# Performance work log

Measured on AMD Instinct MI355X. Metric: run time of the kernel, lower is better.

Reference implementation:

```python
import jax, jax.numpy as jnp
import numpy as np

NUM_QUBITS = 12
BOND_DIM = 8
DIM = 2 ** NUM_QUBITS  # 4096


def setup_inputs() -> dict:
    key = jax.random.key(0)
    k0, k1, k2, k3 = jax.random.split(key, 4)
    core0 = jax.random.normal(k0, (2, BOND_DIM), dtype=jnp.float32) * 0.5
    cores_mid = jax.random.normal(k1, (NUM_QUBITS - 2, BOND_DIM, 2, BOND_DIM), dtype=jnp.float32) * 0.5
    core_last = jax.random.normal(k2, (BOND_DIM, 2), dtype=jnp.float32) * 0.5
    A = jax.random.normal(k3, (DIM, DIM), dtype=jnp.float32)
    H = 0.5 * (A + A.T)  # Hamiltonians are symmetric
    return {"core0": core0, "cores_mid": cores_mid, "core_last": core_last, "H": H}


def _build_state(core0, cores_mid, core_last):
    # Sequential MPS contraction: state grows (2^k, D) site by site.
    state = core0  # (2, D)
    n_mid = cores_mid.shape[0]
    D = core0.shape[1]
    for i in range(n_mid):  # fixed, small layer loop (not a data-dim loop)
        # (S, a) x (a, p, b) -> (S, p, b) -> (S*2, b)
        state = jnp.einsum('sa,apb->spb', state, cores_mid[i]).reshape(-1, D)
    # (S, a) x (a, p) -> flat state vector of length 2^n
    psi = jnp.einsum('sa,ap->sp', state, core_last).reshape(-1)
    return psi


def reference(core0, cores_mid, core_last, H):
    psi = _build_state(core0, cores_mid, core_last)  # (2^n,)
    norm = jnp.dot(psi, psi)
    hpsi = H @ psi
    energy = jnp.dot(psi, hpsi) / norm          # <psi|H|psi>/<psi|psi>
    e2 = jnp.dot(psi, H @ hpsi) / norm          # <psi|H^2|psi>/<psi|psi>
    variance = jnp.maximum(e2 - energy * energy, 0.0)
    return jnp.stack([energy, variance])
```

## Files before the change

kernel.cpp:

```cpp
#include <hip/hip_runtime.h>
#include <hip/hip_bf16.h>


#define DIM 4096
#define BOND 8
#define NMID 10
#define T 128
#define NT (DIM / T)
#define NPAIRS (NT * (NT + 1) / 2)


__global__ __launch_bounds__(256) void build_psi_kernel(
    const float* __restrict__ core0,
    const float* __restrict__ cores_mid,
    const float* __restrict__ core_last,
    float* __restrict__ psi_g,
    float* __restrict__ hpsi_g) {
  __shared__ float c0[16];
  __shared__ float cm[NMID * 128];
  __shared__ float cl[16];

  if (threadIdx.x < 16) {
    c0[threadIdx.x] = core0[threadIdx.x];
    cl[threadIdx.x] = core_last[threadIdx.x];
  }
  for (int j = threadIdx.x; j < NMID * 128; j += 256) cm[j] = cores_mid[j];
  __syncthreads();

  const int idx = blockIdx.x * 256 + threadIdx.x;
  hpsi_g[idx] = 0.f;

  float v[BOND], nv[BOND];
  const int s0 = (idx >> 11) & 1;
#pragma unroll
  for (int a = 0; a < BOND; a++) v[a] = c0[s0 * BOND + a];

#pragma unroll
  for (int i = 0; i < NMID; i++) {
    const int p = (idx >> (10 - i)) & 1;
    const float* M = &cm[i * 128 + p * BOND];
#pragma unroll
    for (int b = 0; b < BOND; b++) nv[b] = v[0] * M[b];
#pragma unroll
    for (int a = 1; a < BOND; a++) {
#pragma unroll
      for (int b = 0; b < BOND; b++) nv[b] += v[a] * M[a * 16 + b];
    }
#pragma unroll
    for (int a = 0; a < BOND; a++) v[a] = nv[a];
  }

  const int pl = idx & 1;
  float ps = 0.f;
#pragma unroll
  for (int a = 0; a < BOND; a++) ps += v[a] * cl[a * 2 + pl];

  psi_g[idx] = ps;
}

__global__ __launch_bounds__(256) void symv_kernel(
    const float* __restrict__ H,
    const float* __restrict__ psi_g,
    float* __restrict__ hpsi_g) {
  int rem = blockIdx.x;
  int bi = 0;
  while (rem >= NT - bi) { rem -= (NT - bi); ++bi; }
  const int bj = bi + rem;
  const bool diag = (bi == bj);

  __shared__ float xI[T], xJ[T], yI_s[T], yJp[4 * T];

  if (threadIdx.x < T) {
    xI[threadIdx.x] = psi_g[bi * T + threadIdx.x];
    xJ[threadIdx.x] = psi_g[bj * T + threadIdx.x];
  }
  __syncthreads();

  const int wave = threadIdx.x >> 6;
  const int lane = threadIdx.x & 63;
  const float* __restrict__ base = H + (size_t)(bi * T) * DIM + bj * T;

  float aJx = 0.f, aJy = 0.f;
  const float pJx = xJ[lane * 2], pJy = xJ[lane * 2 + 1];

#pragma unroll 4
  for (int k = 0; k < T / 4; ++k) {
    const int r = k * 4 + wave;
    const float2 a = *reinterpret_cast<const float2*>(base + (size_t)r * DIM + lane * 2);
    const float xr = xI[r];
    aJx += a.x * xr;
    aJy += a.y * xr;
    float d = a.x * pJx + a.y * pJy;
#pragma unroll
    for (int off = 32; off > 0; off >>= 1) d += __shfl_down(d, off, 64);
    if (lane == 0) yI_s[r] = d;
  }

  yJp[wave * T + lane * 2] = aJx;
  yJp[wave * T + lane * 2 + 1] = aJy;
  __syncthreads();

  if (threadIdx.x < T) {
    atomicAdd(&hpsi_g[bi * T + threadIdx.x], yI_s[threadIdx.x]);
    if (!diag) {
      const float yj = yJp[threadIdx.x] + yJp[T + threadIdx.x] +
                       yJp[2 * T + threadIdx.x] + yJp[3 * T + threadIdx.x];
      atomicAdd(&hpsi_g[bj * T + threadIdx.x], yj);
    }
  }
}

__global__ __launch_bounds__(256) void dots_kernel(
    const float* __restrict__ psi_g,
    const float* __restrict__ hpsi_g,
    float* __restrict__ out) {
  __shared__ double s_n[4], s_ph[4], s_hh[4];
  double n = 0.0, ph = 0.0, hh = 0.0;
  for (int i = threadIdx.x; i < DIM; i += 256) {
    const double p = (double)psi_g[i];
    const double h = (double)hpsi_g[i];
    n += p * p;
    ph += p * h;
    hh += h * h;
  }
#pragma unroll
  for (int off = 32; off > 0; off >>= 1) {
    n += __shfl_down(n, off, 64);
    ph += __shfl_down(ph, off, 64);
    hh += __shfl_down(hh, off, 64);
  }
  const int wave = threadIdx.x >> 6;
  const int lane = threadIdx.x & 63;
  if (lane == 0) { s_n[wave] = n; s_ph[wave] = ph; s_hh[wave] = hh; }
  __syncthreads();
  if (threadIdx.x == 0) {
    double N = 0.0, P = 0.0, HH = 0.0;
#pragma unroll
    for (int w = 0; w < 4; w++) { N += s_n[w]; P += s_ph[w]; HH += s_hh[w]; }
    const double e = P / N;
    const double e2 = HH / N;
    double var = e2 - e * e;
    if (var < 0.0) var = 0.0;
    out[0] = (float)e;
    out[1] = (float)var;
  }
}

extern "C" void kernel_launch(void* const* d_in, const int* in_sizes, int n_in,
                              void* d_out, int out_size, void* d_ws, size_t ws_size,
                              hipStream_t stream) {
  const float* core0 = (const float*)d_in[0];
  const float* cores_mid = (const float*)d_in[1];
  const float* core_last = (const float*)d_in[2];
  const float* H = (const float*)d_in[3];

  float* psi = (float*)d_ws;
  float* hpsi = psi + DIM;

  build_psi_kernel<<<DIM / 256, 256, 0, stream>>>(core0, cores_mid, core_last, psi, hpsi);
  symv_kernel<<<NPAIRS, 256, 0, stream>>>(H, psi, hpsi);
  dots_kernel<<<1, 256, 0, stream>>>(psi, hpsi, (float*)d_out);
}
```

Before: 123.4 us.

## Fuse state build, symmetric matvec and reductions into one cooperative kernel

Merges the three kernels (MPS state build, blocked symmetric matvec, final dot reductions) into a single cooperative launch separated by grid-wide syncs. Each tile block recomputes the psi slices it needs in registers instead of reading them from global memory, and diagonal blocks write psi and zero hpsi. The aim is to remove two kernel launch gaps and the global round trip for psi. In exchange it adds cooperative-launch overhead, grid barrier costs, and redundant psi computation per block.

```diff
diff --git a/kernel.cpp b/kernel.cpp
--- a/kernel.cpp
+++ b/kernel.cpp
@@ -1,5 +1,7 @@
 #include <hip/hip_runtime.h>
-#include <hip/hip_bf16.h>
+#include <hip/hip_cooperative_groups.h>
+
+namespace cg = cooperative_groups;
 
 
 #define DIM 4096
@@ -9,16 +11,25 @@
 #define NT (DIM / T)
 #define NPAIRS (NT * (NT + 1) / 2)
 
-
-__global__ __launch_bounds__(256) void build_psi_kernel(
+__global__ __launch_bounds__(256, 3) void fused_vqe_kernel(
     const float* __restrict__ core0,
     const float* __restrict__ cores_mid,
     const float* __restrict__ core_last,
+    const float* __restrict__ H,
     float* __restrict__ psi_g,
-    float* __restrict__ hpsi_g) {
-  __shared__ float c0[16];
-  __shared__ float cm[NMID * 128];
-  __shared__ float cl[16];
+    float* __restrict__ hpsi_g,
+    float* __restrict__ out) {
+  cg::grid_group grid = cg::this_grid();
+
+  __shared__ float c0[16], cm[NMID * 128], cl[16];
+  __shared__ float xI[T], xJ[T], yI_s[T], yJp[4 * T];
+  __shared__ double sred[12];
+
+  int rem = blockIdx.x;
+  int bi = 0;
+  while (rem >= NT - bi) { rem -= (NT - bi); ++bi; }
+  const int bj = bi + rem;
+  const bool diag = (bi == bj);
 
   if (threadIdx.x < 16) {
     c0[threadIdx.x] = core0[threadIdx.x];
@@ -27,54 +38,43 @@
   for (int j = threadIdx.x; j < NMID * 128; j += 256) cm[j] = cores_mid[j];
   __syncthreads();
 
-  const int idx = blockIdx.x * 256 + threadIdx.x;
-  hpsi_g[idx] = 0.f;
+  {
+    const int local = threadIdx.x & 127;
+    const int slice = (threadIdx.x < 128) ? bi : bj;
+    const int idx = slice * T + local;
 
-  float v[BOND], nv[BOND];
-  const int s0 = (idx >> 11) & 1;
+    float v[BOND], nv[BOND];
+    const int s0 = (idx >> 11) & 1;
 #pragma unroll
-  for (int a = 0; a < BOND; a++) v[a] = c0[s0 * BOND + a];
+    for (int a = 0; a < BOND; a++) v[a] = c0[s0 * BOND + a];
+#pragma unroll
+    for (int i = 0; i < NMID; i++) {
+      const int p = (idx >> (10 - i)) & 1;
+      const float* M = &cm[i * 128 + p * BOND];
+#pragma unroll
+      for (int b = 0; b < BOND; b++) nv[b] = v[0] * M[b];
+#pragma unroll
+      for (int a = 1; a < BOND; a++) {
+#pragma unroll
+        for (int b = 0; b < BOND; b++) nv[b] += v[a] * M[a * 16 + b];
+      }
+#pragma unroll
+      for (int a = 0; a < BOND; a++) v[a] = nv[a];
+    }
+    const int pl = idx & 1;
+    float ps = 0.f;
+#pragma unroll
+    for (int a = 0; a < BOND; a++) ps += v[a] * cl[a * 2 + pl];
 
-#pragma unroll
-  for (int i = 0; i < NMID; i++) {
-    const int p = (idx >> (10 - i)) & 1;
-    const float* M = &cm[i * 128 + p * BOND];
-#pragma unroll
-    for (int b = 0; b < BOND; b++) nv[b] = v[0] * M[b];
-#pragma unroll
-    for (int a = 1; a < BOND; a++) {
-#pragma unroll
-      for (int b = 0; b < BOND; b++) nv[b] += v[a] * M[a * 16 + b];
+    if (threadIdx.x < 128) xI[local] = ps; else xJ[local] = ps;
+
+    if (diag && threadIdx.x < 128) {
+      psi_g[idx] = ps;
+      hpsi_g[idx] = 0.f;
     }
-#pragma unroll
-    for (int a = 0; a < BOND; a++) v[a] = nv[a];
-  }
-
-  const int pl = idx & 1;
-  float ps = 0.f;
-#pragma unroll
-  for (int a = 0; a < BOND; a++) ps += v[a] * cl[a * 2 + pl];
-
-  psi_g[idx] = ps;
-}
-
-__global__ __launch_bounds__(256) void symv_kernel(
-    const float* __restrict__ H,
-    const float* __restrict__ psi_g,
-    float* __restrict__ hpsi_g) {
-  int rem = blockIdx.x;
-  int bi = 0;
-  while (rem >= NT - bi) { rem -= (NT - bi); ++bi; }
-  const int bj = bi + rem;
-  const bool diag = (bi == bj);
-
-  __shared__ float xI[T], xJ[T], yI_s[T], yJp[4 * T];
-
-  if (threadIdx.x < T) {
-    xI[threadIdx.x] = psi_g[bi * T + threadIdx.x];
-    xJ[threadIdx.x] = psi_g[bj * T + threadIdx.x];
   }
   __syncthreads();
+  grid.sync();
 
   const int wave = threadIdx.x >> 6;
   const int lane = threadIdx.x & 63;
@@ -108,41 +108,36 @@
       atomicAdd(&hpsi_g[bj * T + threadIdx.x], yj);
     }
   }
-}
+  grid.sync();
 
-__global__ __launch_bounds__(256) void dots_kernel(
-    const float* __restrict__ psi_g,
-    const float* __restrict__ hpsi_g,
-    float* __restrict__ out) {
-  __shared__ double s_n[4], s_ph[4], s_hh[4];
-  double n = 0.0, ph = 0.0, hh = 0.0;
-  for (int i = threadIdx.x; i < DIM; i += 256) {
-    const double p = (double)psi_g[i];
-    const double h = (double)hpsi_g[i];
-    n += p * p;
-    ph += p * h;
-    hh += h * h;
-  }
+  if (blockIdx.x == 0) {
+    double n = 0.0, ph = 0.0, hh = 0.0;
+    for (int i = threadIdx.x; i < DIM; i += 256) {
+      const double p = (double)psi_g[i];
+      const double h = (double)hpsi_g[i];
+      n += p * p;
+      ph += p * h;
+      hh += h * h;
+    }
 #pragma unroll
-  for (int off = 32; off > 0; off >>= 1) {
-    n += __shfl_down(n, off, 64);
-    ph += __shfl_down(ph, off, 64);
-    hh += __shfl_down(hh, off, 64);
-  }
-  const int wave = threadIdx.x >> 6;
-  const int lane = threadIdx.x & 63;
-  if (lane == 0) { s_n[wave] = n; s_ph[wave] = ph; s_hh[wave] = hh; }
-  __syncthreads();
-  if (threadIdx.x == 0) {
-    double N = 0.0, P = 0.0, HH = 0.0;
+    for (int off = 32; off > 0; off >>= 1) {
+      n += __shfl_down(n, off, 64);
+      ph += __shfl_down(ph, off, 64);
+      hh += __shfl_down(hh, off, 64);
+    }
+    if (lane == 0) { sred[wave] = n; sred[4 + wave] = ph; sred[8 + wave] = hh; }
+    __syncthreads();
+    if (threadIdx.x == 0) {
+      double N = 0.0, P = 0.0, HH = 0.0;
 #pragma unroll
-    for (int w = 0; w < 4; w++) { N += s_n[w]; P += s_ph[w]; HH += s_hh[w]; }
-    const double e = P / N;
-    const double e2 = HH / N;
-    double var = e2 - e * e;
-    if (var < 0.0) var = 0.0;
-    out[0] = (float)e;
-    out[1] = (float)var;
+      for (int w = 0; w < 4; w++) { N += sred[w]; P += sred[4 + w]; HH += sred[8 + w]; }
+      const double e = P / N;
+      const double e2 = HH / N;
+      double var = e2 - e * e;
+      if (var < 0.0) var = 0.0;
+      out[0] = (float)e;
+      out[1] = (float)var;
+    }
   }
 }
 
@@ -156,8 +151,10 @@
 
   float* psi = (float*)d_ws;
   float* hpsi = psi + DIM;
+  float* out = (float*)d_out;
 
-  build_psi_kernel<<<DIM / 256, 256, 0, stream>>>(core0, cores_mid, core_last, psi, hpsi);
-  symv_kernel<<<NPAIRS, 256, 0, stream>>>(H, psi, hpsi);
-  dots_kernel<<<1, 256, 0, stream>>>(psi, hpsi, (float*)d_out);
+  void* args[] = {(void*)&core0, (void*)&cores_mid, (void*)&core_last,
+                  (void*)&H, (void*)&psi, (void*)&hpsi, (void*)&out};
+  hipLaunchCooperativeKernel((const void*)fused_vqe_kernel, dim3(NPAIRS),
+                             dim3(256), args, 0, stream);
 }
```

Result: slower. 228.2 us (+84.9%).
